# Optimization experiments

Measured on AMD Instinct MI355X. Metric: run time of the kernel, lower is better.

## Reference

```python
import jax, jax.numpy as jnp
import numpy as np

C = 512
H_HEADS = 8
HEAD_DIM = C // H_HEADS


def setup_inputs() -> dict:
    key = jax.random.key(0)
    ks = jax.random.split(key, 6)
    B, Hs, Ws = 16, 32, 32
    x = jax.random.normal(ks[0], (B, C, Hs, Ws), dtype=jnp.float32)
    qkv_w = jax.random.normal(ks[1], (3 * C, C), dtype=jnp.float32) * 0.02
    proj_w = jax.random.normal(ks[2], (C, C), dtype=jnp.float32) * 0.02
    proj_b = jnp.zeros((C,), dtype=jnp.float32)
    ln_g = jnp.ones((C,), dtype=jnp.float32)
    ln_b = jnp.zeros((C,), dtype=jnp.float32)
    return {"x": x, "qkv_w": qkv_w, "proj_w": proj_w, "proj_b": proj_b,
            "ln_g": ln_g, "ln_b": ln_b}


def _layernorm(x, g, b, eps=1e-5):
    mu = jnp.mean(x, axis=-1, keepdims=True)
    var = jnp.var(x, axis=-1, keepdims=True)
    return (x - mu) * jax.lax.rsqrt(var + eps) * g + b


def reference(x, qkv_w, proj_w, proj_b, ln_g, ln_b):
    B, Cc, Hs, Ws = x.shape
    N = Hs * Ws
    # (B, N, C)
    x_flat = x.reshape(B, Cc, N).transpose(0, 2, 1)
    x_norm = _layernorm(x_flat, ln_g, ln_b)
    # qkv: torch Linear y = x @ W^T
    qkv = x_norm @ qkv_w.T  # (B, N, 3C)
    qkv = qkv.reshape(B, N, 3, H_HEADS, HEAD_DIM).transpose(2, 0, 3, 1, 4)
    q, k, v = qkv[0], qkv[1], qkv[2]  # (B, h, N, d)
    scale = HEAD_DIM ** -0.5
    attn = jnp.einsum('bhnd,bhmd->bhnm', q, k) * scale
    attn = jax.nn.softmax(attn, axis=-1)
    out = jnp.einsum('bhnm,bhmd->bhnd', attn, v)  # (B, h, N, d)
    out = out.transpose(0, 2, 1, 3).reshape(B, N, Cc)
    out = out @ proj_w.T + proj_b
    out = out + x_flat
    return out.transpose(0, 2, 1).reshape(B, Cc, Hs, Ws)
```

## Files before the change

kernel.cpp:

```cpp
#include <hip/hip_runtime.h>
#include <stdint.h>

typedef unsigned short u16;
typedef __attribute__((ext_vector_type(4))) float f32x4;
typedef __attribute__((ext_vector_type(8))) short s16x8;
typedef __attribute__((ext_vector_type(4))) unsigned short u16x4;
typedef __attribute__((ext_vector_type(8))) unsigned short u16x8;
typedef __attribute__((ext_vector_type(4))) unsigned int u32x4;

__device__ __forceinline__ u16 f2bf(float f) {
  union { float f; uint32_t u; } v; v.f = f;
  uint32_t r = (v.u + 0x7FFFu + ((v.u >> 16) & 1u)) >> 16;
  return (u16)r;
}

__device__ __forceinline__ uint32_t cvtpk(float lo, float hi) {
  uint32_t r;
  asm("v_cvt_pk_bf16_f32 %0, %1, %2" : "=v"(r) : "v"(lo), "v"(hi));
  return r;
}

__device__ __forceinline__ float fexp2(float x) {
#if __has_builtin(__builtin_amdgcn_exp2f)
  return __builtin_amdgcn_exp2f(x);
#else
  float r; asm("v_exp_f32 %0, %1" : "=v"(r) : "v"(x)); return r;
#endif
}

__device__ __forceinline__ void gload_lds16(const void* g, void* l) {
  __builtin_amdgcn_global_load_lds((const __attribute__((address_space(1))) uint32_t*)g,
                                   (__attribute__((address_space(3))) uint32_t*)l, 16, 0, 0);
}

__global__ __launch_bounds__(256) void cvt_kernel(const float* __restrict__ src,
                                                  u16* __restrict__ dst, int n) {
  const int i = (blockIdx.x * 256 + threadIdx.x) * 4;
  if (i < n) {
    f32x4 v = *(const f32x4*)(src + i);
    u16x4 p;
    p[0] = f2bf(v[0]); p[1] = f2bf(v[1]); p[2] = f2bf(v[2]); p[3] = f2bf(v[3]);
    *(u16x4*)(dst + i) = p;
  }
}

__global__ __launch_bounds__(256) void ln_kernel(const float* __restrict__ x,
                                                 const float* __restrict__ lng,
                                                 const float* __restrict__ lnb,
                                                 u16* __restrict__ xn) {
  __shared__ float xt[16][516];
  __shared__ float ps[16][16], pq[16][16];
  __shared__ float smu[16], srs[16];
  const int tid = threadIdx.x;
  const int tok0 = blockIdx.x << 4;
  const int b = tok0 >> 10;
  const int nb = tok0 & 1023;
  const float* xb = x + (size_t)b * 512 * 1024 + nb;
  {
    const int n4 = (tid & 3) * 4;
    const int cr = tid >> 2;
#pragma unroll
    for (int it = 0; it < 8; ++it) {
      const int c = it * 64 + cr;
      f32x4 v = *(const f32x4*)(xb + (size_t)c * 1024 + n4);
      xt[n4 + 0][c] = v[0]; xt[n4 + 1][c] = v[1];
      xt[n4 + 2][c] = v[2]; xt[n4 + 3][c] = v[3];
    }
  }
  __syncthreads();
  {
    const int n = tid & 15, part = tid >> 4;
    float s = 0.f, q = 0.f;
#pragma unroll
    for (int i = 0; i < 8; ++i) {
      f32x4 v = *(const f32x4*)&xt[n][part * 32 + i * 4];
#pragma unroll
      for (int j = 0; j < 4; ++j) { s += v[j]; q += v[j] * v[j]; }
    }
    ps[part][n] = s; pq[part][n] = q;
  }
  __syncthreads();
  if (tid < 16) {
    float s = 0.f, q = 0.f;
#pragma unroll
    for (int p = 0; p < 16; ++p) { s += ps[p][tid]; q += pq[p][tid]; }
    const float mu = s * (1.f / 512.f);
    const float var = q * (1.f / 512.f) - mu * mu;
    smu[tid] = mu; srs[tid] = rsqrtf(var + 1e-5f);
  }
  __syncthreads();
  {
    const int n = tid >> 4, sub = tid & 15;
    const float mu = smu[n], rs = srs[n];
    u16* dst = xn + (size_t)(tok0 + n) * 512;
#pragma unroll
    for (int i = 0; i < 4; ++i) {
      const int c = (sub + 16 * i) * 8;
      f32x4 v0 = *(const f32x4*)&xt[n][c];
      f32x4 v1 = *(const f32x4*)&xt[n][c + 4];
      f32x4 g0 = *(const f32x4*)(lng + c);
      f32x4 g1 = *(const f32x4*)(lng + c + 4);
      f32x4 b0 = *(const f32x4*)(lnb + c);
      f32x4 b1 = *(const f32x4*)(lnb + c + 4);
      union { u32x4 w; u16x8 v; } pk;
      float r0 = (v0[0] - mu) * rs * g0[0] + b0[0];
      float r1 = (v0[1] - mu) * rs * g0[1] + b0[1];
      float r2 = (v0[2] - mu) * rs * g0[2] + b0[2];
      float r3 = (v0[3] - mu) * rs * g0[3] + b0[3];
      float r4 = (v1[0] - mu) * rs * g1[0] + b1[0];
      float r5 = (v1[1] - mu) * rs * g1[1] + b1[1];
      float r6 = (v1[2] - mu) * rs * g1[2] + b1[2];
      float r7 = (v1[3] - mu) * rs * g1[3] + b1[3];
      pk.w[0] = cvtpk(r0, r1); pk.w[1] = cvtpk(r2, r3);
      pk.w[2] = cvtpk(r4, r5); pk.w[3] = cvtpk(r6, r7);
      *(u16x8*)(dst + c) = pk.v;
    }
  }
}

template <int EPI>
__global__ __launch_bounds__(256) void gemm_bt(const u16* __restrict__ A,
                                               const u16* __restrict__ Bw,
                                               void* __restrict__ Cout,
                                               u16* __restrict__ vt,
                                               const float* __restrict__ bias,
                                               const float* __restrict__ resid,
                                               int M, int N, int K,
                                               long bsz, long csz, long rsz) {
  __shared__ u16 Al[2][128 * 32];
  __shared__ u16 Bl[2][128 * 32];
  const int tid = threadIdx.x;
  const int w = tid >> 6, lane = tid & 63;
  const int lg = lane >> 4, l15 = lane & 15;
  const int wr = w >> 1, wc = w & 1;
  int m0, n0, z;
  if (EPI == 0) {
    const int blk = blockIdx.x;
    const int c = blk & 7, j = blk >> 3;
    m0 = (c * 16 + j / 12) * 128;
    n0 = (j % 12) * 128;
    z = 0;
  } else {
    m0 = blockIdx.x * 128; n0 = blockIdx.y * 128; z = blockIdx.z;
  }
  const u16* Bz = Bw + (size_t)z * bsz;
  const float* Rz = (EPI == 1) ? resid + (size_t)z * rsz : nullptr;

  f32x4 acc[4][4];
#pragma unroll
  for (int i = 0; i < 4; ++i)
#pragma unroll
    for (int j = 0; j < 4; ++j) acc[i][j] = (f32x4){0.f, 0.f, 0.f, 0.f};

  const int sr = lane >> 2, sch = (lane & 3) * 8;
  const u16* ap = A + (size_t)(m0 + w * 32 + sr) * K + sch;
  const u16* bp = Bz + (size_t)(n0 + w * 32 + sr) * K + sch;

  auto stage = [&](int buf) {
    gload_lds16(ap,          &Al[buf][(w * 32 + 0) * 32]);
    gload_lds16(ap + 16 * K, &Al[buf][(w * 32 + 16) * 32]);
    gload_lds16(bp,          &Bl[buf][(w * 32 + 0) * 32]);
    gload_lds16(bp + 16 * K, &Bl[buf][(w * 32 + 16) * 32]);
    ap += 32; bp += 32;
  };
  auto compute = [&](int buf) {
    s16x8 af[4], bfr[4];
#pragma unroll
    for (int mi = 0; mi < 4; ++mi)
      af[mi] = *(const s16x8*)&Al[buf][(wr * 64 + mi * 16 + l15) * 32 + lg * 8];
#pragma unroll
    for (int ni = 0; ni < 4; ++ni)
      bfr[ni] = *(const s16x8*)&Bl[buf][(wc * 64 + ni * 16 + l15) * 32 + lg * 8];
#pragma unroll
    for (int mi = 0; mi < 4; ++mi)
#pragma unroll
      for (int ni = 0; ni < 4; ++ni)
        acc[mi][ni] = __builtin_amdgcn_mfma_f32_16x16x32_bf16(af[mi], bfr[ni], acc[mi][ni], 0, 0, 0);
  };

  const int nk2 = K >> 6;
  stage(0);
#pragma unroll 1
  for (int it = 0; it < nk2 - 1; ++it) {
    stage(1);
    asm volatile("s_waitcnt vmcnt(4)" ::: "memory");
    __builtin_amdgcn_s_barrier();
    asm volatile("" ::: "memory");
    compute(0);
    asm volatile("" ::: "memory");
    __builtin_amdgcn_s_barrier();
    stage(0);
    asm volatile("s_waitcnt vmcnt(4)" ::: "memory");
    __builtin_amdgcn_s_barrier();
    asm volatile("" ::: "memory");
    compute(1);
    asm volatile("" ::: "memory");
    __builtin_amdgcn_s_barrier();
  }
  stage(1);
  asm volatile("s_waitcnt vmcnt(4)" ::: "memory");
  __builtin_amdgcn_s_barrier();
  asm volatile("" ::: "memory");
  compute(0);
  asm volatile("" ::: "memory");
  __builtin_amdgcn_s_barrier();
  asm volatile("s_waitcnt vmcnt(0)" ::: "memory");
  __builtin_amdgcn_s_barrier();
  asm volatile("" ::: "memory");
  compute(1);

  if (EPI == 0) {
    if (n0 < 512) {
      const float ce = 0.125f * 1.44269504f;
#pragma unroll
      for (int mi = 0; mi < 4; ++mi)
#pragma unroll
        for (int ni = 0; ni < 4; ++ni)
#pragma unroll
          for (int r = 0; r < 4; ++r) acc[mi][ni][r] *= ce;
    }
    u16* C = (u16*)Cout;
    if (n0 < 1024) {
#pragma unroll
      for (int mi = 0; mi < 4; ++mi)
#pragma unroll
        for (int ni = 0; ni < 4; ++ni) {
          const int col = n0 + wc * 64 + ni * 16 + l15;
          const int row = m0 + wr * 64 + mi * 16 + lg * 4;
          const uint32_t w0 = cvtpk(acc[mi][ni][0], acc[mi][ni][1]);
          const uint32_t w1 = cvtpk(acc[mi][ni][2], acc[mi][ni][3]);
          C[(size_t)(row + 0) * 1024 + col] = (u16)w0;
          C[(size_t)(row + 1) * 1024 + col] = (u16)(w0 >> 16);
          C[(size_t)(row + 2) * 1024 + col] = (u16)w1;
          C[(size_t)(row + 3) * 1024 + col] = (u16)(w1 >> 16);
        }
    } else {
#pragma unroll
      for (int mi = 0; mi < 4; ++mi)
#pragma unroll
        for (int ni = 0; ni < 4; ++ni) {
          const int vcol = n0 - 1024 + wc * 64 + ni * 16 + l15;
          const int hh = vcol >> 6, d = vcol & 63;
          const int token = m0 + wr * 64 + mi * 16 + lg * 4;
          const int b = token >> 10, g15 = (token >> 6) & 15;
          const int p = 32 * (mi >> 1) + 8 * lg + 4 * (mi & 1);
          union { uint32_t w[2]; u16x4 v; } pk;
          pk.w[0] = cvtpk(acc[mi][ni][0], acc[mi][ni][1]);
          pk.w[1] = cvtpk(acc[mi][ni][2], acc[mi][ni][3]);
          *(u16x4*)&vt[(size_t)((b * 8 + hh) * 64 + d) * 1024 + g15 * 64 + p] = pk.v;
        }
    }
  } else {
    float* C = (float*)Cout + (size_t)z * csz;
#pragma unroll
    for (int mi = 0; mi < 4; ++mi)
#pragma unroll
      for (int ni = 0; ni < 4; ++ni) {
        const int col = n0 + wc * 64 + ni * 16 + l15;
#pragma unroll
        for (int r = 0; r < 4; ++r) {
          const int row = m0 + wr * 64 + mi * 16 + lg * 4 + r;
          C[(size_t)row * N + col] = acc[mi][ni][r] + bias[row] + Rz[(size_t)row * N + col];
        }
      }
  }
}

__global__ __launch_bounds__(256, 4) void attn_kernel(const u16* __restrict__ qk,
                                                      const u16* __restrict__ vt,
                                                      u16* __restrict__ ao) {
  __shared__ union {
    struct { u16 K[2][64 * 64]; u16 V[2][64 * 64]; } s;
    struct { float O[4][16][68]; float ls[4 * 32]; } e;
  } sm;
  const int tid = threadIdx.x;
  const int w = tid >> 6, lane = tid & 63;
  const int lg = lane >> 4, l15 = lane & 15;
  const int blk = blockIdx.x;
  const int qb = (blk >> 3) & 7;
  const int bh = (blk & 7) | ((blk >> 6) << 3);
  const int b = bh >> 3, h = bh & 7;
  const size_t qbase = (size_t)b * 1024 * 1024;
  const size_t vbase = (size_t)bh * 64 * 1024;
  const int qtok0 = qb * 128 + w * 32;

  s16x8 qf[2][2];
#pragma unroll
  for (int s = 0; s < 2; ++s)
#pragma unroll
    for (int qg = 0; qg < 2; ++qg)
      qf[s][qg] = *(const s16x8*)(qk + qbase + (size_t)(qtok0 + qg * 16 + l15) * 1024 +
                                  h * 64 + lg * 8 + 32 * s);

  f32x4 o[2][4];
  f32x4 lacc[2];
#pragma unroll
  for (int qg = 0; qg < 2; ++qg) {
    lacc[qg] = (f32x4){0.f, 0.f, 0.f, 0.f};
#pragma unroll
    for (int db = 0; db < 4; ++db) o[qg][db] = (f32x4){0.f, 0.f, 0.f, 0.f};
  }
  s16x8 ones;
#pragma unroll
  for (int j = 0; j < 8; ++j) ones[j] = (short)0x3F80;

  const int srr = lane >> 3, sch = lane & 7;
  const int row0 = w * 16 + srr, row1 = row0 + 8;
  const u16* kp0 = qk + qbase + (size_t)row0 * 1024 + 512 + h * 64 + ((sch ^ (row0 & 7)) * 8);
  const u16* kp1 = qk + qbase + (size_t)row1 * 1024 + 512 + h * 64 + ((sch ^ (row1 & 7)) * 8);
  const u16* vp0 = vt + vbase + (size_t)row0 * 1024 + ((sch ^ (row0 & 7)) * 8);
  const u16* vp1 = vt + vbase + (size_t)row1 * 1024 + ((sch ^ (row1 & 7)) * 8);

  auto stage = [&](int buf) {
    gload_lds16(kp0, &sm.s.K[buf][(w * 16 + 0) * 64]);
    gload_lds16(kp1, &sm.s.K[buf][(w * 16 + 8) * 64]);
    gload_lds16(vp0, &sm.s.V[buf][(w * 16 + 0) * 64]);
    gload_lds16(vp1, &sm.s.V[buf][(w * 16 + 8) * 64]);
    kp0 += 64 * 1024; kp1 += 64 * 1024;
    vp0 += 64; vp1 += 64;
  };

  auto compute = [&](int buf) {
    f32x4 st[4][2];
#pragma unroll
    for (int kg = 0; kg < 4; ++kg)
#pragma unroll
      for (int qg = 0; qg < 2; ++qg) st[kg][qg] = (f32x4){0.f, 0.f, 0.f, 0.f};
    __builtin_amdgcn_s_setprio(1);
#pragma unroll
    for (int s = 0; s < 2; ++s)
#pragma unroll
      for (int kg = 0; kg < 4; ++kg) {
        const int row = kg * 16 + l15;
        s16x8 kf = *(const s16x8*)&sm.s.K[buf][row * 64 +
                                              ((lg * 8 + 32 * s) ^ ((row & 7) << 3))];
#pragma unroll
        for (int qg = 0; qg < 2; ++qg)
          st[kg][qg] = __builtin_amdgcn_mfma_f32_16x16x32_bf16(kf, qf[s][qg], st[kg][qg], 0, 0, 0);
      }
    __builtin_amdgcn_s_setprio(0);

    s16x8 pa[2][2];
#pragma unroll
    for (int qg = 0; qg < 2; ++qg) {
      float pv[16];
#pragma unroll
      for (int kg = 0; kg < 4; ++kg)
#pragma unroll
        for (int r = 0; r < 4; ++r)
          pv[kg * 4 + r] = fexp2(st[kg][qg][r]);
#pragma unroll
      for (int kh = 0; kh < 2; ++kh) {
        union { u32x4 wd; s16x8 v; } pk;
        pk.wd[0] = cvtpk(pv[8 * kh + 0], pv[8 * kh + 1]);
        pk.wd[1] = cvtpk(pv[8 * kh + 2], pv[8 * kh + 3]);
        pk.wd[2] = cvtpk(pv[8 * kh + 4], pv[8 * kh + 5]);
        pk.wd[3] = cvtpk(pv[8 * kh + 6], pv[8 * kh + 7]);
        pa[qg][kh] = pk.v;
      }
    }

    __builtin_amdgcn_s_setprio(1);
#pragma unroll
    for (int kh = 0; kh < 2; ++kh) {
#pragma unroll
      for (int db = 0; db < 4; ++db) {
        const int d = db * 16 + l15;
        s16x8 vf = *(const s16x8*)&sm.s.V[buf][d * 64 +
                                               ((kh * 32 + lg * 8) ^ ((d & 7) << 3))];
#pragma unroll
        for (int qg = 0; qg < 2; ++qg)
          o[qg][db] = __builtin_amdgcn_mfma_f32_16x16x32_bf16(pa[qg][kh], vf, o[qg][db], 0, 0, 0);
      }
#pragma unroll
      for (int qg = 0; qg < 2; ++qg)
        lacc[qg] = __builtin_amdgcn_mfma_f32_16x16x32_bf16(pa[qg][kh], ones, lacc[qg], 0, 0, 0);
    }
    __builtin_amdgcn_s_setprio(0);
  };

  stage(0);
#pragma unroll 1
  for (int it = 0; it < 7; ++it) {
    stage(1);
    asm volatile("s_waitcnt vmcnt(4)" ::: "memory");
    __builtin_amdgcn_s_barrier();
    asm volatile("" ::: "memory");
    compute(0);
    asm volatile("" ::: "memory");
    __builtin_amdgcn_s_barrier();
    stage(0);
    asm volatile("s_waitcnt vmcnt(4)" ::: "memory");
    __builtin_amdgcn_s_barrier();
    asm volatile("" ::: "memory");
    compute(1);
    asm volatile("" ::: "memory");
    __builtin_amdgcn_s_barrier();
  }
  stage(1);
  asm volatile("s_waitcnt vmcnt(4)" ::: "memory");
  __builtin_amdgcn_s_barrier();
  asm volatile("" ::: "memory");
  compute(0);
  asm volatile("" ::: "memory");
  __builtin_amdgcn_s_barrier();
  asm volatile("s_waitcnt vmcnt(0)" ::: "memory");
  __builtin_amdgcn_s_barrier();
  asm volatile("" ::: "memory");
  compute(1);

  __syncthreads();
  if (l15 == 0) {
#pragma unroll
    for (int qg = 0; qg < 2; ++qg)
#pragma unroll
      for (int r = 0; r < 4; ++r)
        sm.e.ls[w * 32 + qg * 16 + lg * 4 + r] = lacc[qg][r];
  }
#pragma unroll
  for (int half = 0; half < 2; ++half) {
#pragma unroll
    for (int db = 0; db < 4; ++db)
#pragma unroll
      for (int r = 0; r < 4; ++r)
        sm.e.O[w][lg * 4 + r][db * 16 + l15] = o[half][db][r];
    __syncthreads();
    {
      const int q = lane & 15, dh = lane >> 4;
      const float inv = 1.0f / sm.e.ls[w * 32 + half * 16 + q];
      u16* dst = ao + (size_t)(b * 1024 + qtok0 + half * 16 + q) * 512 + h * 64 + dh * 16;
      f32x4 v0 = *(const f32x4*)&sm.e.O[w][q][dh * 16 + 0];
      f32x4 v1 = *(const f32x4*)&sm.e.O[w][q][dh * 16 + 4];
      f32x4 v2 = *(const f32x4*)&sm.e.O[w][q][dh * 16 + 8];
      f32x4 v3 = *(const f32x4*)&sm.e.O[w][q][dh * 16 + 12];
      union { u32x4 wd; u16x8 v; } p0, p1;
      p0.wd[0] = cvtpk(v0[0] * inv, v0[1] * inv);
      p0.wd[1] = cvtpk(v0[2] * inv, v0[3] * inv);
      p0.wd[2] = cvtpk(v1[0] * inv, v1[1] * inv);
      p0.wd[3] = cvtpk(v1[2] * inv, v1[3] * inv);
      p1.wd[0] = cvtpk(v2[0] * inv, v2[1] * inv);
      p1.wd[1] = cvtpk(v2[2] * inv, v2[3] * inv);
      p1.wd[2] = cvtpk(v3[0] * inv, v3[1] * inv);
      p1.wd[3] = cvtpk(v3[2] * inv, v3[3] * inv);
      *(u16x8*)(dst + 0) = p0.v;
      *(u16x8*)(dst + 8) = p1.v;
    }
    __syncthreads();
  }
}

extern "C" void kernel_launch(void* const* d_in, const int* in_sizes, int n_in,
                              void* d_out, int out_size, void* d_ws, size_t ws_size,
                              hipStream_t stream) {
  const float* x      = (const float*)d_in[0];
  const float* qkv_w  = (const float*)d_in[1];
  const float* proj_w = (const float*)d_in[2];
  const float* proj_b = (const float*)d_in[3];
  const float* ln_g   = (const float*)d_in[4];
  const float* ln_b   = (const float*)d_in[5];
  float* out = (float*)d_out;

  char* ws = (char*)d_ws;
  u16* xn  = (u16*)ws;
  u16* qk  = (u16*)(ws + (size_t)16 * 1024 * 1024);
  u16* vt  = (u16*)(ws + (size_t)48 * 1024 * 1024);
  u16* ao  = (u16*)(ws + (size_t)64 * 1024 * 1024);
  u16* qw  = (u16*)(ws + (size_t)80 * 1024 * 1024);
  u16* pw  = qw + 1536 * 512;

  cvt_kernel<<<768, 256, 0, stream>>>(qkv_w, qw, 1536 * 512);
  cvt_kernel<<<256, 256, 0, stream>>>(proj_w, pw, 512 * 512);
  ln_kernel<<<1024, 256, 0, stream>>>(x, ln_g, ln_b, xn);
  gemm_bt<0><<<1536, 256, 0, stream>>>(xn, qw, qk, vt, nullptr, nullptr,
                                       16384, 1024, 512, 0, 0, 0);
  attn_kernel<<<1024, 256, 0, stream>>>(qk, vt, ao);
  gemm_bt<1><<<dim3(4, 8, 16), 256, 0, stream>>>(pw, ao, out, nullptr, proj_b, x,
                                                 512, 1024, 512,
                                                 (long)1024 * 512, (long)512 * 1024,
                                                 (long)512 * 1024);
}
```

Before: 222.8 us.

## Split attention block across eight waves with sixteen queries each

The attention kernel now launches 512 threads per block (eight waves), each handling 16 query rows instead of 32, while keeping 128 queries per block. Each wave stages one row of K and V per tile instead of two, and the epilogue runs in a single pass. The aim is more waves in flight to hide latency and fewer registers per wave. In exchange, each K/V tile read from LDS now feeds half as many MFMAs per wave, which lowers per-wave reuse and raises LDS read traffic per unit of work.

```diff
diff --git a/kernel.cpp b/kernel.cpp
--- a/kernel.cpp
+++ b/kernel.cpp
@@ -266,12 +266,12 @@
   }
 }
 
-__global__ __launch_bounds__(256, 4) void attn_kernel(const u16* __restrict__ qk,
+__global__ __launch_bounds__(512, 8) void attn_kernel(const u16* __restrict__ qk,
                                                       const u16* __restrict__ vt,
                                                       u16* __restrict__ ao) {
   __shared__ union {
     struct { u16 K[2][64 * 64]; u16 V[2][64 * 64]; } s;
-    struct { float O[4][16][68]; float ls[4 * 32]; } e;
+    struct { float O[8][16][66]; float ls[128]; } e;
   } sm;
   const int tid = threadIdx.x;
   const int w = tid >> 6, lane = tid & 63;
@@ -282,50 +282,39 @@
   const int b = bh >> 3, h = bh & 7;
   const size_t qbase = (size_t)b * 1024 * 1024;
   const size_t vbase = (size_t)bh * 64 * 1024;
-  const int qtok0 = qb * 128 + w * 32;
-
-  s16x8 qf[2][2];
+  const int qtok0 = qb * 128 + w * 16;
+
+  s16x8 qf[2];
 #pragma unroll
   for (int s = 0; s < 2; ++s)
-#pragma unroll
-    for (int qg = 0; qg < 2; ++qg)
-      qf[s][qg] = *(const s16x8*)(qk + qbase + (size_t)(qtok0 + qg * 16 + l15) * 1024 +
-                                  h * 64 + lg * 8 + 32 * s);
-
-  f32x4 o[2][4];
-  f32x4 lacc[2];
-#pragma unroll
-  for (int qg = 0; qg < 2; ++qg) {
-    lacc[qg] = (f32x4){0.f, 0.f, 0.f, 0.f};
-#pragma unroll
-    for (int db = 0; db < 4; ++db) o[qg][db] = (f32x4){0.f, 0.f, 0.f, 0.f};
-  }
+    qf[s] = *(const s16x8*)(qk + qbase + (size_t)(qtok0 + l15) * 1024 +
+                            h * 64 + lg * 8 + 32 * s);
+
+  f32x4 o[4];
+  f32x4 lacc;
+  lacc = (f32x4){0.f, 0.f, 0.f, 0.f};
+#pragma unroll
+  for (int db = 0; db < 4; ++db) o[db] = (f32x4){0.f, 0.f, 0.f, 0.f};
   s16x8 ones;
 #pragma unroll
   for (int j = 0; j < 8; ++j) ones[j] = (short)0x3F80;
 
   const int srr = lane >> 3, sch = lane & 7;
-  const int row0 = w * 16 + srr, row1 = row0 + 8;
-  const u16* kp0 = qk + qbase + (size_t)row0 * 1024 + 512 + h * 64 + ((sch ^ (row0 & 7)) * 8);
-  const u16* kp1 = qk + qbase + (size_t)row1 * 1024 + 512 + h * 64 + ((sch ^ (row1 & 7)) * 8);
-  const u16* vp0 = vt + vbase + (size_t)row0 * 1024 + ((sch ^ (row0 & 7)) * 8);
-  const u16* vp1 = vt + vbase + (size_t)row1 * 1024 + ((sch ^ (row1 & 7)) * 8);
+  const int row0 = w * 8 + srr;
+  const u16* kp = qk + qbase + (size_t)row0 * 1024 + 512 + h * 64 + ((sch ^ (row0 & 7)) * 8);
+  const u16* vp = vt + vbase + (size_t)row0 * 1024 + ((sch ^ (row0 & 7)) * 8);
 
   auto stage = [&](int buf) {
-    gload_lds16(kp0, &sm.s.K[buf][(w * 16 + 0) * 64]);
-    gload_lds16(kp1, &sm.s.K[buf][(w * 16 + 8) * 64]);
-    gload_lds16(vp0, &sm.s.V[buf][(w * 16 + 0) * 64]);
-    gload_lds16(vp1, &sm.s.V[buf][(w * 16 + 8) * 64]);
-    kp0 += 64 * 1024; kp1 += 64 * 1024;
-    vp0 += 64; vp1 += 64;
+    gload_lds16(kp, &sm.s.K[buf][(w * 8) * 64]);
+    gload_lds16(vp, &sm.s.V[buf][(w * 8) * 64]);
+    kp += 64 * 1024;
+    vp += 64;
   };
 
   auto compute = [&](int buf) {
-    f32x4 st[4][2];
-#pragma unroll
-    for (int kg = 0; kg < 4; ++kg)
-#pragma unroll
-      for (int qg = 0; qg < 2; ++qg) st[kg][qg] = (f32x4){0.f, 0.f, 0.f, 0.f};
+    f32x4 st[4];
+#pragma unroll
+    for (int kg = 0; kg < 4; ++kg) st[kg] = (f32x4){0.f, 0.f, 0.f, 0.f};
     __builtin_amdgcn_s_setprio(1);
 #pragma unroll
     for (int s = 0; s < 2; ++s)
@@ -334,30 +323,25 @@
         const int row = kg * 16 + l15;
         s16x8 kf = *(const s16x8*)&sm.s.K[buf][row * 64 +
                                               ((lg * 8 + 32 * s) ^ ((row & 7) << 3))];
-#pragma unroll
-        for (int qg = 0; qg < 2; ++qg)
-          st[kg][qg] = __builtin_amdgcn_mfma_f32_16x16x32_bf16(kf, qf[s][qg], st[kg][qg], 0, 0, 0);
+        st[kg] = __builtin_amdgcn_mfma_f32_16x16x32_bf16(kf, qf[s], st[kg], 0, 0, 0);
       }
     __builtin_amdgcn_s_setprio(0);
 
-    s16x8 pa[2][2];
-#pragma unroll
-    for (int qg = 0; qg < 2; ++qg) {
-      float pv[16];
-#pragma unroll
-      for (int kg = 0; kg < 4; ++kg)
-#pragma unroll
-        for (int r = 0; r < 4; ++r)
-          pv[kg * 4 + r] = fexp2(st[kg][qg][r]);
-#pragma unroll
-      for (int kh = 0; kh < 2; ++kh) {
-        union { u32x4 wd; s16x8 v; } pk;
-        pk.wd[0] = cvtpk(pv[8 * kh + 0], pv[8 * kh + 1]);
-        pk.wd[1] = cvtpk(pv[8 * kh + 2], pv[8 * kh + 3]);
-        pk.wd[2] = cvtpk(pv[8 * kh + 4], pv[8 * kh + 5]);
-        pk.wd[3] = cvtpk(pv[8 * kh + 6], pv[8 * kh + 7]);
-        pa[qg][kh] = pk.v;
-      }
+    float pv[16];
+#pragma unroll
+    for (int kg = 0; kg < 4; ++kg)
+#pragma unroll
+      for (int r = 0; r < 4; ++r)
+        pv[kg * 4 + r] = fexp2(st[kg][r]);
+    s16x8 pa[2];
+#pragma unroll
+    for (int kh = 0; kh < 2; ++kh) {
+      union { u32x4 wd; s16x8 v; } pk;
+      pk.wd[0] = cvtpk(pv[8 * kh + 0], pv[8 * kh + 1]);
+      pk.wd[1] = cvtpk(pv[8 * kh + 2], pv[8 * kh + 3]);
+      pk.wd[2] = cvtpk(pv[8 * kh + 4], pv[8 * kh + 5]);
+      pk.wd[3] = cvtpk(pv[8 * kh + 6], pv[8 * kh + 7]);
+      pa[kh] = pk.v;
     }
 
     __builtin_amdgcn_s_setprio(1);
@@ -368,13 +352,9 @@
         const int d = db * 16 + l15;
         s16x8 vf = *(const s16x8*)&sm.s.V[buf][d * 64 +
                                                ((kh * 32 + lg * 8) ^ ((d & 7) << 3))];
-#pragma unroll
-        for (int qg = 0; qg < 2; ++qg)
-          o[qg][db] = __builtin_amdgcn_mfma_f32_16x16x32_bf16(pa[qg][kh], vf, o[qg][db], 0, 0, 0);
+        o[db] = __builtin_amdgcn_mfma_f32_16x16x32_bf16(pa[kh], vf, o[db], 0, 0, 0);
       }
-#pragma unroll
-      for (int qg = 0; qg < 2; ++qg)
-        lacc[qg] = __builtin_amdgcn_mfma_f32_16x16x32_bf16(pa[qg][kh], ones, lacc[qg], 0, 0, 0);
+      lacc = __builtin_amdgcn_mfma_f32_16x16x32_bf16(pa[kh], ones, lacc, 0, 0, 0);
     }
     __builtin_amdgcn_s_setprio(0);
   };
@@ -383,14 +363,14 @@
 #pragma unroll 1
   for (int it = 0; it < 7; ++it) {
     stage(1);
-    asm volatile("s_waitcnt vmcnt(4)" ::: "memory");
+    asm volatile("s_waitcnt vmcnt(2)" ::: "memory");
     __builtin_amdgcn_s_barrier();
     asm volatile("" ::: "memory");
     compute(0);
     asm volatile("" ::: "memory");
     __builtin_amdgcn_s_barrier();
     stage(0);
-    asm volatile("s_waitcnt vmcnt(4)" ::: "memory");
+    asm volatile("s_waitcnt vmcnt(2)" ::: "memory");
     __builtin_amdgcn_s_barrier();
     asm volatile("" ::: "memory");
     compute(1);
@@ -398,7 +378,7 @@
     __builtin_amdgcn_s_barrier();
   }
   stage(1);
-  asm volatile("s_waitcnt vmcnt(4)" ::: "memory");
+  asm volatile("s_waitcnt vmcnt(2)" ::: "memory");
   __builtin_amdgcn_s_barrier();
   asm volatile("" ::: "memory");
   compute(0);
@@ -412,40 +392,34 @@
   __syncthreads();
   if (l15 == 0) {
 #pragma unroll
-    for (int qg = 0; qg < 2; ++qg)
-#pragma unroll
-      for (int r = 0; r < 4; ++r)
-        sm.e.ls[w * 32 + qg * 16 + lg * 4 + r] = lacc[qg][r];
-  }
-#pragma unroll
-  for (int half = 0; half < 2; ++half) {
-#pragma unroll
-    for (int db = 0; db < 4; ++db)
-#pragma unroll
-      for (int r = 0; r < 4; ++r)
-        sm.e.O[w][lg * 4 + r][db * 16 + l15] = o[half][db][r];
-    __syncthreads();
-    {
-      const int q = lane & 15, dh = lane >> 4;
-      const float inv = 1.0f / sm.e.ls[w * 32 + half * 16 + q];
-      u16* dst = ao + (size_t)(b * 1024 + qtok0 + half * 16 + q) * 512 + h * 64 + dh * 16;
-      f32x4 v0 = *(const f32x4*)&sm.e.O[w][q][dh * 16 + 0];
-      f32x4 v1 = *(const f32x4*)&sm.e.O[w][q][dh * 16 + 4];
-      f32x4 v2 = *(const f32x4*)&sm.e.O[w][q][dh * 16 + 8];
-      f32x4 v3 = *(const f32x4*)&sm.e.O[w][q][dh * 16 + 12];
-      union { u32x4 wd; u16x8 v; } p0, p1;
-      p0.wd[0] = cvtpk(v0[0] * inv, v0[1] * inv);
-      p0.wd[1] = cvtpk(v0[2] * inv, v0[3] * inv);
-      p0.wd[2] = cvtpk(v1[0] * inv, v1[1] * inv);
-      p0.wd[3] = cvtpk(v1[2] * inv, v1[3] * inv);
-      p1.wd[0] = cvtpk(v2[0] * inv, v2[1] * inv);
-      p1.wd[1] = cvtpk(v2[2] * inv, v2[3] * inv);
-      p1.wd[2] = cvtpk(v3[0] * inv, v3[1] * inv);
-      p1.wd[3] = cvtpk(v3[2] * inv, v3[3] * inv);
-      *(u16x8*)(dst + 0) = p0.v;
-      *(u16x8*)(dst + 8) = p1.v;
-    }
-    __syncthreads();
+    for (int r = 0; r < 4; ++r)
+      sm.e.ls[w * 16 + lg * 4 + r] = lacc[r];
+  }
+#pragma unroll
+  for (int db = 0; db < 4; ++db)
+#pragma unroll
+    for (int r = 0; r < 4; ++r)
+      sm.e.O[w][lg * 4 + r][db * 16 + l15] = o[db][r];
+  __syncthreads();
+  {
+    const int q = lane & 15, dh = lane >> 4;
+    const float inv = 1.0f / sm.e.ls[w * 16 + q];
+    u16* dst = ao + (size_t)(b * 1024 + qtok0 + q) * 512 + h * 64 + dh * 16;
+    f32x4 v0 = *(const f32x4*)&sm.e.O[w][q][dh * 16 + 0];
+    f32x4 v1 = *(const f32x4*)&sm.e.O[w][q][dh * 16 + 4];
+    f32x4 v2 = *(const f32x4*)&sm.e.O[w][q][dh * 16 + 8];
+    f32x4 v3 = *(const f32x4*)&sm.e.O[w][q][dh * 16 + 12];
+    union { u32x4 wd; u16x8 v; } p0, p1;
+    p0.wd[0] = cvtpk(v0[0] * inv, v0[1] * inv);
+    p0.wd[1] = cvtpk(v0[2] * inv, v0[3] * inv);
+    p0.wd[2] = cvtpk(v1[0] * inv, v1[1] * inv);
+    p0.wd[3] = cvtpk(v1[2] * inv, v1[3] * inv);
+    p1.wd[0] = cvtpk(v2[0] * inv, v2[1] * inv);
+    p1.wd[1] = cvtpk(v2[2] * inv, v2[3] * inv);
+    p1.wd[2] = cvtpk(v3[0] * inv, v3[1] * inv);
+    p1.wd[3] = cvtpk(v3[2] * inv, v3[3] * inv);
+    *(u16x8*)(dst + 0) = p0.v;
+    *(u16x8*)(dst + 8) = p1.v;
   }
 }
 
@@ -473,7 +447,7 @@
   ln_kernel<<<1024, 256, 0, stream>>>(x, ln_g, ln_b, xn);
   gemm_bt<0><<<1536, 256, 0, stream>>>(xn, qw, qk, vt, nullptr, nullptr,
                                        16384, 1024, 512, 0, 0, 0);
-  attn_kernel<<<1024, 256, 0, stream>>>(qk, vt, ao);
+  attn_kernel<<<1024, 512, 0, stream>>>(qk, vt, ao);
   gemm_bt<1><<<dim3(4, 8, 16), 256, 0, stream>>>(pw, ao, out, nullptr, proj_b, x,
                                                  512, 1024, 512,
                                                  (long)1024 * 512, (long)512 * 1024,
```

Measured after the change: 278.0 us. +24.8%, slower.

## Stage QK-GEMM epilogue through LDS and switch attention K/V loads to register prefetch

Applied to the files above, without the earlier changes.

The QK GEMM epilogue now writes bf16 results into a padded LDS tile and then stores full rows with 16-byte coalesced writes, replacing scattered 2-byte global stores. The attention kernel replaces direct global-to-LDS loads with an XOR swizzle by register-staged loads into padded (stride 72) LDS tiles. The next tile's loads are issued before compute and written to LDS afterward, which drops one barrier per stage. This raises register pressure in the attention kernel, which has launch bounds of 4 blocks, and adds LDS write traffic plus two barriers to the GEMM epilogue.

```diff
diff --git a/kernel.cpp b/kernel.cpp
--- a/kernel.cpp
+++ b/kernel.cpp
@@ -127,8 +127,10 @@
                                                const float* __restrict__ resid,
                                                int M, int N, int K,
                                                long bsz, long csz, long rsz) {
-  __shared__ u16 Al[2][128 * 32];
-  __shared__ u16 Bl[2][128 * 32];
+  __shared__ union {
+    struct { u16 A[2][128 * 32]; u16 B[2][128 * 32]; } m;
+    u16 t[128 * 136];
+  } sg;
   const int tid = threadIdx.x;
   const int w = tid >> 6, lane = tid & 63;
   const int lg = lane >> 4, l15 = lane & 15;
@@ -157,20 +159,20 @@
   const u16* bp = Bz + (size_t)(n0 + w * 32 + sr) * K + sch;
 
   auto stage = [&](int buf) {
-    gload_lds16(ap,          &Al[buf][(w * 32 + 0) * 32]);
-    gload_lds16(ap + 16 * K, &Al[buf][(w * 32 + 16) * 32]);
-    gload_lds16(bp,          &Bl[buf][(w * 32 + 0) * 32]);
-    gload_lds16(bp + 16 * K, &Bl[buf][(w * 32 + 16) * 32]);
+    gload_lds16(ap,          &sg.m.A[buf][(w * 32 + 0) * 32]);
+    gload_lds16(ap + 16 * K, &sg.m.A[buf][(w * 32 + 16) * 32]);
+    gload_lds16(bp,          &sg.m.B[buf][(w * 32 + 0) * 32]);
+    gload_lds16(bp + 16 * K, &sg.m.B[buf][(w * 32 + 16) * 32]);
     ap += 32; bp += 32;
   };
   auto compute = [&](int buf) {
     s16x8 af[4], bfr[4];
 #pragma unroll
     for (int mi = 0; mi < 4; ++mi)
-      af[mi] = *(const s16x8*)&Al[buf][(wr * 64 + mi * 16 + l15) * 32 + lg * 8];
+      af[mi] = *(const s16x8*)&sg.m.A[buf][(wr * 64 + mi * 16 + l15) * 32 + lg * 8];
 #pragma unroll
     for (int ni = 0; ni < 4; ++ni)
-      bfr[ni] = *(const s16x8*)&Bl[buf][(wc * 64 + ni * 16 + l15) * 32 + lg * 8];
+      bfr[ni] = *(const s16x8*)&sg.m.B[buf][(wc * 64 + ni * 16 + l15) * 32 + lg * 8];
 #pragma unroll
     for (int mi = 0; mi < 4; ++mi)
 #pragma unroll
@@ -210,30 +212,28 @@
   compute(1);
 
   if (EPI == 0) {
-    if (n0 < 512) {
-      const float ce = 0.125f * 1.44269504f;
-#pragma unroll
-      for (int mi = 0; mi < 4; ++mi)
-#pragma unroll
-        for (int ni = 0; ni < 4; ++ni)
-#pragma unroll
-          for (int r = 0; r < 4; ++r) acc[mi][ni][r] *= ce;
-    }
     u16* C = (u16*)Cout;
     if (n0 < 1024) {
+      const float ce = (n0 < 512) ? 0.125f * 1.44269504f : 1.0f;
+      __syncthreads();
 #pragma unroll
       for (int mi = 0; mi < 4; ++mi)
 #pragma unroll
         for (int ni = 0; ni < 4; ++ni) {
-          const int col = n0 + wc * 64 + ni * 16 + l15;
-          const int row = m0 + wr * 64 + mi * 16 + lg * 4;
-          const uint32_t w0 = cvtpk(acc[mi][ni][0], acc[mi][ni][1]);
-          const uint32_t w1 = cvtpk(acc[mi][ni][2], acc[mi][ni][3]);
-          C[(size_t)(row + 0) * 1024 + col] = (u16)w0;
-          C[(size_t)(row + 1) * 1024 + col] = (u16)(w0 >> 16);
-          C[(size_t)(row + 2) * 1024 + col] = (u16)w1;
-          C[(size_t)(row + 3) * 1024 + col] = (u16)(w1 >> 16);
+          const int colb = wc * 64 + ni * 16 + l15;
+#pragma unroll
+          for (int r = 0; r < 4; ++r) {
+            const int rowb = wr * 64 + mi * 16 + lg * 4 + r;
+            sg.t[rowb * 136 + colb] = (u16)cvtpk(acc[mi][ni][r] * ce, 0.f);
+          }
         }
+      __syncthreads();
+#pragma unroll
+      for (int itr = 0; itr < 8; ++itr) {
+        const int rowb = itr * 16 + (tid >> 4);
+        u16x8 v8 = *(const u16x8*)&sg.t[rowb * 136 + (tid & 15) * 8];
+        *(u16x8*)(C + (size_t)(m0 + rowb) * 1024 + n0 + (tid & 15) * 8) = v8;
+      }
     } else {
 #pragma unroll
       for (int mi = 0; mi < 4; ++mi)
@@ -270,7 +270,7 @@
                                                       const u16* __restrict__ vt,
                                                       u16* __restrict__ ao) {
   __shared__ union {
-    struct { u16 K[2][64 * 64]; u16 V[2][64 * 64]; } s;
+    struct { u16 K[2][64 * 72]; u16 V[2][64 * 72]; } s;
     struct { float O[4][16][68]; float ls[4 * 32]; } e;
   } sm;
   const int tid = threadIdx.x;
@@ -305,20 +305,27 @@
   for (int j = 0; j < 8; ++j) ones[j] = (short)0x3F80;
 
   const int srr = lane >> 3, sch = lane & 7;
-  const int row0 = w * 16 + srr, row1 = row0 + 8;
-  const u16* kp0 = qk + qbase + (size_t)row0 * 1024 + 512 + h * 64 + ((sch ^ (row0 & 7)) * 8);
-  const u16* kp1 = qk + qbase + (size_t)row1 * 1024 + 512 + h * 64 + ((sch ^ (row1 & 7)) * 8);
-  const u16* vp0 = vt + vbase + (size_t)row0 * 1024 + ((sch ^ (row0 & 7)) * 8);
-  const u16* vp1 = vt + vbase + (size_t)row1 * 1024 + ((sch ^ (row1 & 7)) * 8);
-
-  auto stage = [&](int buf) {
-    gload_lds16(kp0, &sm.s.K[buf][(w * 16 + 0) * 64]);
-    gload_lds16(kp1, &sm.s.K[buf][(w * 16 + 8) * 64]);
-    gload_lds16(vp0, &sm.s.V[buf][(w * 16 + 0) * 64]);
-    gload_lds16(vp1, &sm.s.V[buf][(w * 16 + 8) * 64]);
+  const int row0 = w * 16 + srr;
+  const u16* kp0 = qk + qbase + (size_t)row0 * 1024 + 512 + h * 64 + sch * 8;
+  const u16* kp1 = kp0 + 8 * 1024;
+  const u16* vp0 = vt + vbase + (size_t)row0 * 1024 + sch * 8;
+  const u16* vp1 = vp0 + 8 * 1024;
+
+  u32x4 kr0, kr1, vr0, vr1;
+  auto loadr = [&]() {
+    kr0 = *(const u32x4*)kp0; kr1 = *(const u32x4*)kp1;
+    vr0 = *(const u32x4*)vp0; vr1 = *(const u32x4*)vp1;
     kp0 += 64 * 1024; kp1 += 64 * 1024;
     vp0 += 64; vp1 += 64;
   };
+  const int woff0 = (w * 16 + srr) * 72 + sch * 8;
+  const int woff1 = (w * 16 + 8 + srr) * 72 + sch * 8;
+  auto writeb = [&](int buf) {
+    *(u32x4*)&sm.s.K[buf][woff0] = kr0;
+    *(u32x4*)&sm.s.K[buf][woff1] = kr1;
+    *(u32x4*)&sm.s.V[buf][woff0] = vr0;
+    *(u32x4*)&sm.s.V[buf][woff1] = vr1;
+  };
 
   auto compute = [&](int buf) {
     f32x4 st[4][2];
@@ -332,8 +339,7 @@
 #pragma unroll
       for (int kg = 0; kg < 4; ++kg) {
         const int row = kg * 16 + l15;
-        s16x8 kf = *(const s16x8*)&sm.s.K[buf][row * 64 +
-                                              ((lg * 8 + 32 * s) ^ ((row & 7) << 3))];
+        s16x8 kf = *(const s16x8*)&sm.s.K[buf][row * 72 + lg * 8 + 32 * s];
 #pragma unroll
         for (int qg = 0; qg < 2; ++qg)
           st[kg][qg] = __builtin_amdgcn_mfma_f32_16x16x32_bf16(kf, qf[s][qg], st[kg][qg], 0, 0, 0);
@@ -366,8 +372,7 @@
 #pragma unroll
       for (int db = 0; db < 4; ++db) {
         const int d = db * 16 + l15;
-        s16x8 vf = *(const s16x8*)&sm.s.V[buf][d * 64 +
-                                               ((kh * 32 + lg * 8) ^ ((d & 7) << 3))];
+        s16x8 vf = *(const s16x8*)&sm.s.V[buf][d * 72 + kh * 32 + lg * 8];
 #pragma unroll
         for (int qg = 0; qg < 2; ++qg)
           o[qg][db] = __builtin_amdgcn_mfma_f32_16x16x32_bf16(pa[qg][kh], vf, o[qg][db], 0, 0, 0);
@@ -379,32 +384,29 @@
     __builtin_amdgcn_s_setprio(0);
   };
 
-  stage(0);
+  loadr(); writeb(0);
+  asm volatile("s_waitcnt lgkmcnt(0)" ::: "memory");
+  __builtin_amdgcn_s_barrier();
+  asm volatile("" ::: "memory");
 #pragma unroll 1
   for (int it = 0; it < 7; ++it) {
-    stage(1);
-    asm volatile("s_waitcnt vmcnt(4)" ::: "memory");
-    __builtin_amdgcn_s_barrier();
-    asm volatile("" ::: "memory");
+    loadr();
     compute(0);
-    asm volatile("" ::: "memory");
-    __builtin_amdgcn_s_barrier();
-    stage(0);
-    asm volatile("s_waitcnt vmcnt(4)" ::: "memory");
-    __builtin_amdgcn_s_barrier();
-    asm volatile("" ::: "memory");
+    writeb(1);
+    asm volatile("s_waitcnt lgkmcnt(0)" ::: "memory");
+    __builtin_amdgcn_s_barrier();
+    asm volatile("" ::: "memory");
+    loadr();
     compute(1);
-    asm volatile("" ::: "memory");
-    __builtin_amdgcn_s_barrier();
-  }
-  stage(1);
-  asm volatile("s_waitcnt vmcnt(4)" ::: "memory");
-  __builtin_amdgcn_s_barrier();
-  asm volatile("" ::: "memory");
+    writeb(0);
+    asm volatile("s_waitcnt lgkmcnt(0)" ::: "memory");
+    __builtin_amdgcn_s_barrier();
+    asm volatile("" ::: "memory");
+  }
+  loadr();
   compute(0);
-  asm volatile("" ::: "memory");
-  __builtin_amdgcn_s_barrier();
-  asm volatile("s_waitcnt vmcnt(0)" ::: "memory");
+  writeb(1);
+  asm volatile("s_waitcnt lgkmcnt(0)" ::: "memory");
   __builtin_amdgcn_s_barrier();
   asm volatile("" ::: "memory");
   compute(1);
```

Result: slower. 232.6 us (+4.4%).
